# Performance work log

Hardware: AMD Instinct MI355X
Metric: run time of the kernel (lower is better)

The kernel has to match this reference:

```python
import jax, jax.numpy as jnp
import numpy as np

N_NODES = 100000
N_EDGES = 3200000
NUM_FEATURES = 512
LATENT_DIM = 64
HIDDEN = 2 * LATENT_DIM


def gcn_conv(x, src, dst, deg_inv_sqrt, W, b, n_nodes):
    # GCNConv: out = D^{-1/2} (A+I) D^{-1/2} X W + b  (transform first, then aggregate)
    h = x @ W  # [N, out]
    norm = deg_inv_sqrt[src] * deg_inv_sqrt[dst]  # [E]
    msg = h[src] * norm[:, None]  # gather + scale
    out = jax.ops.segment_sum(msg, dst, num_segments=n_nodes)
    return out + b


def setup_inputs() -> dict:
    key = jax.random.key(0)
    ks = jax.random.split(key, 8)
    features = jax.random.normal(ks[0], (N_NODES, NUM_FEATURES), dtype=jnp.float32)
    edge_index = jax.random.randint(ks[1], (2, N_EDGES), 0, N_NODES, dtype=jnp.int64)
    # Glorot-ish params
    W1 = jax.random.normal(ks[2], (NUM_FEATURES, HIDDEN), dtype=jnp.float32) / np.sqrt(NUM_FEATURES)
    b1 = jnp.zeros((HIDDEN,), dtype=jnp.float32)
    Wm = jax.random.normal(ks[3], (HIDDEN, LATENT_DIM), dtype=jnp.float32) / np.sqrt(HIDDEN)
    bm = jnp.zeros((LATENT_DIM,), dtype=jnp.float32)
    Wv = jax.random.normal(ks[4], (HIDDEN, LATENT_DIM), dtype=jnp.float32) / np.sqrt(HIDDEN)
    bv = jnp.zeros((LATENT_DIM,), dtype=jnp.float32)
    return {"features": features, "edge_index": edge_index,
            "W1": W1, "b1": b1, "Wm": Wm, "bm": bm, "Wv": Wv, "bv": bv}


def reference(features, edge_index, W1, b1, Wm, bm, Wv, bv):
    n = features.shape[0]
    loop = jnp.arange(n, dtype=edge_index.dtype)
    src = jnp.concatenate([edge_index[0], loop])  # add self-loops
    dst = jnp.concatenate([edge_index[1], loop])
    deg = jax.ops.segment_sum(jnp.ones_like(dst, dtype=features.dtype), dst, num_segments=n)
    deg_inv_sqrt = jnp.where(deg > 0, jax.lax.rsqrt(deg), 0.0)

    h = jax.nn.relu(gcn_conv(features, src, dst, deg_inv_sqrt, W1, b1, n))
    mean = gcn_conv(h, src, dst, deg_inv_sqrt, Wm, bm, n)
    var = gcn_conv(h, src, dst, deg_inv_sqrt, Wv, bv, n)
    return (mean, var)
```

## Files before the change

### kernel.cpp

```cpp
#include <hip/hip_runtime.h>

#define N_FEAT 512
#define HID 128
#define LAT 64

#define NB 98
#define BSHIFT 10
#define BS 1024
#define CAP 34816
#define CHUNK 4096

__device__ __forceinline__ unsigned short f2bf(float f) {
    unsigned u = __float_as_uint(f);
    return (unsigned short)((u + 0x7FFFu + ((u >> 16) & 1u)) >> 16);
}
__device__ __forceinline__ float bf2f(unsigned short h) {
    return __uint_as_float(((unsigned)h) << 16);
}

__global__ __launch_bounds__(256) void bin_kernel(const int* __restrict__ src,
                                                  const int* __restrict__ dst,
                                                  int* __restrict__ gcursor,
                                                  uint2* __restrict__ binned, int E) {
    __shared__ int hist[NB];
    __shared__ int basel[NB];
    __shared__ int gbase[NB];
    __shared__ int cursor[NB];
    __shared__ uint2 staged[CHUNK];
    int tid = threadIdx.x;
    int e0 = blockIdx.x * CHUNK;
    int nE = min(CHUNK, E - e0);
    if (nE <= 0) return;
    for (int i = tid; i < NB; i += 256) hist[i] = 0;
    __syncthreads();
    for (int i = tid; i < nE; i += 256) {
        int d = dst[e0 + i];
        atomicAdd(&hist[d >> BSHIFT], 1);
    }
    __syncthreads();
    if (tid < NB) basel[tid] = hist[tid];
    __syncthreads();
    for (int off = 1; off < NB; off <<= 1) {
        int x = (tid >= off && tid < NB) ? basel[tid - off] : 0;
        __syncthreads();
        if (tid < NB) basel[tid] += x;
        __syncthreads();
    }
    if (tid < NB) {
        int c = hist[tid];
        basel[tid] -= c;
        gbase[tid] = (c > 0) ? atomicAdd(&gcursor[tid], c) : 0;
        cursor[tid] = basel[tid];
    }
    __syncthreads();
    for (int i = tid; i < nE; i += 256) {
        int s = src[e0 + i];
        int d = dst[e0 + i];
        int b = d >> BSHIFT;
        int pos = atomicAdd(&cursor[b], 1);
        staged[pos] = make_uint2((unsigned)s, (unsigned)d);
    }
    __syncthreads();
    for (int i = tid; i < nE; i += 256) {
        uint2 e = staged[i];
        int b = (int)(e.y >> BSHIFT);
        int ofs = gbase[b] + (i - basel[b]);
        if (ofs < CAP) binned[(size_t)b * CAP + ofs] = e;
    }
}

__global__ __launch_bounds__(1024) void build_a_kernel(const uint2* __restrict__ binned,
                                                       const int* __restrict__ gcursor,
                                                       int* __restrict__ counts,
                                                       float* __restrict__ dis,
                                                       int* __restrict__ offsets, int N) {
    __shared__ int nh[BS];
    __shared__ int pref[BS];
    int b = blockIdx.x;
    int tid = threadIdx.x;
    int nEdges = min(gcursor[b], CAP);
    const uint2* rgn = binned + (size_t)b * CAP;
    nh[tid] = 0;
    __syncthreads();
    for (int i = tid; i < nEdges; i += 1024)
        atomicAdd(&nh[rgn[i].y & (BS - 1)], 1);
    __syncthreads();
    int v = nh[tid];
    pref[tid] = v;
    __syncthreads();
    for (int off = 1; off < BS; off <<= 1) {
        int x = (tid >= off) ? pref[tid - off] : 0;
        __syncthreads();
        pref[tid] += x;
        __syncthreads();
    }
    int excl = pref[tid] - v;
    int node = (b << BSHIFT) + tid;
    if (node < N) {
        counts[node] = v;
        dis[node] = rsqrtf((float)(v + 1));
        offsets[node] = b * CAP + excl;
    }
}

__global__ __launch_bounds__(1024) void build_b_kernel(const uint2* __restrict__ binned,
                                                       const int* __restrict__ gcursor,
                                                       const int* __restrict__ offsets,
                                                       const float* __restrict__ dis,
                                                       int2* __restrict__ pairs, int N) {
    __shared__ int cur[BS];
    int b = blockIdx.x;
    int tid = threadIdx.x;
    int nEdges = min(gcursor[b], CAP);
    const uint2* rgn = binned + (size_t)b * CAP;
    int node = (b << BSHIFT) + tid;
    cur[tid] = (node < N) ? offsets[node] : 0;
    __syncthreads();
    for (int i = tid; i < nEdges; i += 1024) {
        uint2 e = rgn[i];
        int pos = atomicAdd(&cur[e.y & (BS - 1)], 1);
        float ws = dis[e.x];
        pairs[pos] = make_int2((int)e.x, __float_as_int(ws));
    }
}

__global__ __launch_bounds__(256) void wsplit_kernel(const float* __restrict__ W,
                                                     unsigned short* __restrict__ WhT,
                                                     unsigned short* __restrict__ WlT) {
    int i = blockIdx.x * 256 + threadIdx.x;
    if (i >= N_FEAT * HID) return;
    int k = i >> 7;
    int n = i & 127;
    float w = W[i];
    unsigned short h = f2bf(w);
    float r = w - bf2f(h);
    WhT[(size_t)n * N_FEAT + k] = h;
    WlT[(size_t)n * N_FEAT + k] = f2bf(r);
}

typedef __attribute__((ext_vector_type(8))) short bf16x8;
typedef __attribute__((ext_vector_type(4))) float f32x4;

#define GM 128
#define GK 32
#define LDA 40

__global__ __launch_bounds__(256) void gemm1_mfma(const float* __restrict__ X,
                                                  const unsigned short* __restrict__ WhT,
                                                  const unsigned short* __restrict__ WlT,
                                                  unsigned short* __restrict__ Tb, int M) {
    __shared__ unsigned short Ah[GM][LDA];
    __shared__ unsigned short Al[GM][LDA];
    __shared__ unsigned short Bh[HID][LDA];
    __shared__ unsigned short Bl[HID][LDA];

    int tid = threadIdx.x;
    int row = tid >> 1;
    int c0 = (tid & 1) * 16;

    int row_g = blockIdx.x * GM + row;
    if (row_g > M - 1) row_g = M - 1;
    const float* xbase = X + (size_t)row_g * N_FEAT;
    const unsigned short* whb = WhT + (size_t)row * N_FEAT;
    const unsigned short* wlb = WlT + (size_t)row * N_FEAT;

    int wid = tid >> 6, lane = tid & 63;
    int wm = wid >> 1, wn = wid & 1;
    int lm = lane & 15;
    int lk8 = (lane >> 4) * 8;

    f32x4 acc[4][4];
    #pragma unroll
    for (int i = 0; i < 4; ++i)
        #pragma unroll
        for (int j = 0; j < 4; ++j) acc[i][j] = (f32x4){0.f, 0.f, 0.f, 0.f};

    float4 xv0 = *(const float4*)(xbase + c0);
    float4 xv1 = *(const float4*)(xbase + c0 + 4);
    float4 xv2 = *(const float4*)(xbase + c0 + 8);
    float4 xv3 = *(const float4*)(xbase + c0 + 12);
    uint4 bhv0 = *(const uint4*)(whb + c0);
    uint4 bhv1 = *(const uint4*)(whb + c0 + 8);
    uint4 blv0 = *(const uint4*)(wlb + c0);
    uint4 blv1 = *(const uint4*)(wlb + c0 + 8);

    for (int k0 = 0; k0 < N_FEAT; k0 += GK) {
        __syncthreads();
        {
            float xs[16] = {xv0.x, xv0.y, xv0.z, xv0.w, xv1.x, xv1.y, xv1.z, xv1.w,
                            xv2.x, xv2.y, xv2.z, xv2.w, xv3.x, xv3.y, xv3.z, xv3.w};
            unsigned short* arow = &Ah[row][c0];
            unsigned short* lrow = &Al[row][c0];
            #pragma unroll
            for (int j = 0; j < 16; j += 2) {
                unsigned short h0 = f2bf(xs[j]);
                unsigned short h1 = f2bf(xs[j + 1]);
                float r0 = xs[j] - bf2f(h0);
                float r1 = xs[j + 1] - bf2f(h1);
                *(unsigned*)&arow[j] = (unsigned)h0 | ((unsigned)h1 << 16);
                *(unsigned*)&lrow[j] = (unsigned)f2bf(r0) | ((unsigned)f2bf(r1) << 16);
            }
            *(uint4*)&Bh[row][c0]     = bhv0;
            *(uint4*)&Bh[row][c0 + 8] = bhv1;
            *(uint4*)&Bl[row][c0]     = blv0;
            *(uint4*)&Bl[row][c0 + 8] = blv1;
        }
        __syncthreads();
        if (k0 + GK < N_FEAT) {
            const float* xp = xbase + k0 + GK + c0;
            xv0 = *(const float4*)(xp);
            xv1 = *(const float4*)(xp + 4);
            xv2 = *(const float4*)(xp + 8);
            xv3 = *(const float4*)(xp + 12);
            bhv0 = *(const uint4*)(whb + k0 + GK + c0);
            bhv1 = *(const uint4*)(whb + k0 + GK + c0 + 8);
            blv0 = *(const uint4*)(wlb + k0 + GK + c0);
            blv1 = *(const uint4*)(wlb + k0 + GK + c0 + 8);
        }
        bf16x8 ah[4], al[4], bh[4], bl[4];
        #pragma unroll
        for (int i = 0; i < 4; ++i) {
            ah[i] = *(const bf16x8*)&Ah[wm * 64 + i * 16 + lm][lk8];
            al[i] = *(const bf16x8*)&Al[wm * 64 + i * 16 + lm][lk8];
            bh[i] = *(const bf16x8*)&Bh[wn * 64 + i * 16 + lm][lk8];
            bl[i] = *(const bf16x8*)&Bl[wn * 64 + i * 16 + lm][lk8];
        }
        #pragma unroll
        for (int i = 0; i < 4; ++i)
            #pragma unroll
            for (int j = 0; j < 4; ++j) {
                acc[i][j] = __builtin_amdgcn_mfma_f32_16x16x32_bf16(ah[i], bh[j], acc[i][j], 0, 0, 0);
                acc[i][j] = __builtin_amdgcn_mfma_f32_16x16x32_bf16(al[i], bh[j], acc[i][j], 0, 0, 0);
                acc[i][j] = __builtin_amdgcn_mfma_f32_16x16x32_bf16(ah[i], bl[j], acc[i][j], 0, 0, 0);
            }
    }

    int orow0 = blockIdx.x * GM + wm * 64 + (lane >> 4) * 4;
    int ocol0 = wn * 64 + lm;
    #pragma unroll
    for (int i = 0; i < 4; ++i)
        #pragma unroll
        for (int j = 0; j < 4; ++j)
            #pragma unroll
            for (int r = 0; r < 4; ++r) {
                int orow = orow0 + i * 16 + r;
                if (orow < M)
                    Tb[(size_t)orow * HID + ocol0 + j * 16] = f2bf(acc[i][j][r]);
            }
}

template <bool RELU_BIAS, bool OUT_BF16>
__global__ __launch_bounds__(256) void agg_kernel(const unsigned short* __restrict__ Tb,
                                                  const int2* __restrict__ pairs,
                                                  const int* __restrict__ offsets,
                                                  const int* __restrict__ counts,
                                                  const float* __restrict__ dis,
                                                  const float* __restrict__ bias,
                                                  void* __restrict__ out, int n) {
    int tid = threadIdx.x;
    int half = tid >> 5;
    int lane = tid & 31;
    int i = blockIdx.x * 8 + half;
    if (i >= n) return;
    float di = dis[i];
    int beg = offsets[i];
    int cnt = counts[i];
    const int2* ep = pairs + beg;
    ushort4 self = ((const ushort4*)(Tb + (size_t)i * HID))[lane];
    float4 acc;
    acc.x = di * bf2f(self.x); acc.y = di * bf2f(self.y);
    acc.z = di * bf2f(self.z); acc.w = di * bf2f(self.w);
    if (cnt > 0) {
        int cm1 = cnt - 1;
        int s[8]; float w[8];
        #pragma unroll
        for (int u = 0; u < 8; ++u) {
            int2 p = ep[min(u, cm1)];
            s[u] = p.x;
            w[u] = (u <= cm1) ? __int_as_float(p.y) : 0.f;
        }
        for (int j = 0; j < cnt; j += 8) {
            ushort4 v[8];
            #pragma unroll
            for (int u = 0; u < 8; ++u)
                v[u] = ((const ushort4*)(Tb + (size_t)s[u] * HID))[lane];
            int jn = j + 8;
            int sN[8]; float wN[8];
            #pragma unroll
            for (int u = 0; u < 8; ++u) {
                int2 p = ep[min(jn + u, cm1)];
                sN[u] = p.x;
                wN[u] = (jn + u <= cm1) ? __int_as_float(p.y) : 0.f;
            }
            #pragma unroll
            for (int u = 0; u < 8; ++u) {
                acc.x += w[u] * bf2f(v[u].x); acc.y += w[u] * bf2f(v[u].y);
                acc.z += w[u] * bf2f(v[u].z); acc.w += w[u] * bf2f(v[u].w);
            }
            #pragma unroll
            for (int u = 0; u < 8; ++u) { s[u] = sN[u]; w[u] = wN[u]; }
        }
    }
    acc.x *= di; acc.y *= di; acc.z *= di; acc.w *= di;
    if (RELU_BIAS) {
        float4 bv = ((const float4*)bias)[lane];
        acc.x = fmaxf(acc.x + bv.x, 0.f);
        acc.y = fmaxf(acc.y + bv.y, 0.f);
        acc.z = fmaxf(acc.z + bv.z, 0.f);
        acc.w = fmaxf(acc.w + bv.w, 0.f);
    }
    if (OUT_BF16) {
        ushort4 o = {f2bf(acc.x), f2bf(acc.y), f2bf(acc.z), f2bf(acc.w)};
        ((ushort4*)((unsigned short*)out + (size_t)i * HID))[lane] = o;
    } else {
        ((float4*)((float*)out + (size_t)i * HID))[lane] = acc;
    }
}

#define BM 64
#define BN 128
#define BK 16
__global__ __launch_bounds__(256) void gemm2_kernel(const float* __restrict__ G,
                                                    const float* __restrict__ Wm,
                                                    const float* __restrict__ bm,
                                                    const float* __restrict__ Wv,
                                                    const float* __restrict__ bv,
                                                    float* __restrict__ outm,
                                                    float* __restrict__ outv, int M) {
    __shared__ float As[BM][BK + 1];
    __shared__ float Bs[BK][BN];
    int tid = threadIdx.x;
    int block_m = blockIdx.x * BM;
    int tx = tid & 15;
    int ty = tid >> 4;

    int a_row = tid >> 2;
    int a_k4 = (tid & 3) << 2;
    int a_row_g = block_m + a_row;
    int a_row_c = a_row_g < M ? a_row_g : (M - 1);
    int b_row = tid >> 5;
    int b_col = (tid & 31) << 2;
    const float* Wsel = (b_col < 64) ? (Wm + b_col) : (Wv + (b_col - 64));

    float acc[4][8];
    #pragma unroll
    for (int i = 0; i < 4; ++i)
        #pragma unroll
        for (int j = 0; j < 8; ++j) acc[i][j] = 0.f;

    for (int k0 = 0; k0 < HID; k0 += BK) {
        float4 av = *(const float4*)&G[(size_t)a_row_c * HID + k0 + a_k4];
        float4 bv0 = *(const float4*)&Wsel[(size_t)(k0 + b_row) * LAT];
        float4 bv1 = *(const float4*)&Wsel[(size_t)(k0 + b_row + 8) * LAT];
        As[a_row][a_k4 + 0] = av.x; As[a_row][a_k4 + 1] = av.y;
        As[a_row][a_k4 + 2] = av.z; As[a_row][a_k4 + 3] = av.w;
        *(float4*)&Bs[b_row][b_col] = bv0;
        *(float4*)&Bs[b_row + 8][b_col] = bv1;
        __syncthreads();
        #pragma unroll
        for (int k = 0; k < BK; ++k) {
            float a[4];
            #pragma unroll
            for (int i = 0; i < 4; ++i) a[i] = As[ty * 4 + i][k];
            float4 bq0 = *(const float4*)&Bs[k][tx * 8];
            float4 bq1 = *(const float4*)&Bs[k][tx * 8 + 4];
            float bb[8] = {bq0.x, bq0.y, bq0.z, bq0.w, bq1.x, bq1.y, bq1.z, bq1.w};
            #pragma unroll
            for (int i = 0; i < 4; ++i)
                #pragma unroll
                for (int j = 0; j < 8; ++j) acc[i][j] += a[i] * bb[j];
        }
        __syncthreads();
    }

    int col0 = tx * 8;
    float* outsel = (col0 < 64) ? (outm + col0) : (outv + (col0 - 64));
    const float* bsel = (col0 < 64) ? (bm + col0) : (bv + (col0 - 64));
    float4 bb0 = *(const float4*)&bsel[0];
    float4 bb1 = *(const float4*)&bsel[4];
    #pragma unroll
    for (int i = 0; i < 4; ++i) {
        int row = block_m + ty * 4 + i;
        if (row < M) {
            float4 o0 = {acc[i][0] + bb0.x, acc[i][1] + bb0.y, acc[i][2] + bb0.z, acc[i][3] + bb0.w};
            float4 o1 = {acc[i][4] + bb1.x, acc[i][5] + bb1.y, acc[i][6] + bb1.z, acc[i][7] + bb1.w};
            *(float4*)&outsel[(size_t)row * LAT] = o0;
            *(float4*)&outsel[(size_t)row * LAT + 4] = o1;
        }
    }
}

extern "C" void kernel_launch(void* const* d_in, const int* in_sizes, int n_in,
                              void* d_out, int out_size, void* d_ws, size_t ws_size,
                              hipStream_t stream) {
    const float* X  = (const float*)d_in[0];
    const int* edge = (const int*)d_in[1];
    const float* W1 = (const float*)d_in[2];
    const float* b1 = (const float*)d_in[3];
    const float* Wm = (const float*)d_in[4];
    const float* bm = (const float*)d_in[5];
    const float* Wv = (const float*)d_in[6];
    const float* bv = (const float*)d_in[7];

    int N = in_sizes[0] / N_FEAT;
    int E = in_sizes[1] / 2;
    const int* srcp = edge;
    const int* dstp = edge + E;

    char* w = (char*)d_ws;
    size_t off = 0;
    auto alloc = [&](size_t bytes) -> void* {
        void* p = w + off;
        off = (off + bytes + 511) & ~(size_t)511;
        return p;
    };
    float* dis    = (float*)alloc((size_t)N * 4);
    int* counts   = (int*)alloc((size_t)N * 4);
    int* offsets  = (int*)alloc((size_t)N * 4);
    int* gcursor  = (int*)alloc((size_t)NB * 4);
    int2* pairs   = (int2*)alloc((size_t)NB * CAP * 8);
    unsigned short* tb = (unsigned short*)alloc((size_t)N * HID * 2);
    unsigned short* hb = (unsigned short*)alloc((size_t)N * HID * 2);
    unsigned short* whT = (unsigned short*)alloc((size_t)N_FEAT * HID * 2);
    unsigned short* wlT = (unsigned short*)alloc((size_t)N_FEAT * HID * 2);
    float* g      = (float*)alloc((size_t)N * HID * 4);
    uint2* binned = (uint2*)g;

    hipMemsetAsync(gcursor, 0, (size_t)NB * 4, stream);
    int nChunks = (E + CHUNK - 1) / CHUNK;
    bin_kernel<<<nChunks, 256, 0, stream>>>(srcp, dstp, gcursor, binned, E);
    build_a_kernel<<<NB, 1024, 0, stream>>>(binned, gcursor, counts, dis, offsets, N);
    build_b_kernel<<<NB, 1024, 0, stream>>>(binned, gcursor, offsets, dis, pairs, N);

    wsplit_kernel<<<(N_FEAT * HID + 255) / 256, 256, 0, stream>>>(W1, whT, wlT);
    gemm1_mfma<<<(N + GM - 1) / GM, 256, 0, stream>>>(X, whT, wlT, tb, N);
    agg_kernel<true, true><<<(N + 7) / 8, 256, 0, stream>>>(tb, pairs, offsets, counts, dis, b1, hb, N);
    agg_kernel<false, false><<<(N + 7) / 8, 256, 0, stream>>>(hb, pairs, offsets, counts, dis, nullptr, g, N);

    float* outm = (float*)d_out;
    float* outv = outm + (size_t)N * LAT;
    gemm2_kernel<<<(N + BM - 1) / BM, 256, 0, stream>>>(g, Wm, bm, Wv, bv, outm, outv, N);
}
```

Measured before the change: 764.5 us.

## Use split-bf16 MFMA for second GEMM and widen aggregation loads to 16 bytes

Replaces the fp32 SIMT second GEMM with an MFMA kernel that takes its inputs as bf16 hi/lo pairs and uses three MFMA products to approximate fp32 accuracy. The second aggregation now writes split bf16 hi/lo outputs instead of fp32, which keeps the intermediate the same size while feeding the MFMA kernel directly. Aggregation switches to 16 lanes per node with 8-element (16-byte) gathers, which halves the number of gather instructions per row. The cost is an extra small weight-split kernel, and the split-bf16 scheme carries some precision risk.

```diff
diff --git a/kernel.cpp b/kernel.cpp
--- a/kernel.cpp
+++ b/kernel.cpp
@@ -17,6 +17,10 @@
 __device__ __forceinline__ float bf2f(unsigned short h) {
     return __uint_as_float(((unsigned)h) << 16);
 }
+
+typedef __attribute__((ext_vector_type(8))) short bf16x8;
+typedef __attribute__((ext_vector_type(4))) float f32x4;
+typedef __attribute__((ext_vector_type(8))) unsigned short u16x8;
 
 __global__ __launch_bounds__(256) void bin_kernel(const int* __restrict__ src,
                                                   const int* __restrict__ dst,
@@ -138,8 +142,20 @@
     WlT[(size_t)n * N_FEAT + k] = f2bf(r);
 }
 
-typedef __attribute__((ext_vector_type(8))) short bf16x8;
-typedef __attribute__((ext_vector_type(4))) float f32x4;
+__global__ __launch_bounds__(256) void wsplit2_kernel(const float* __restrict__ Wm,
+                                                      const float* __restrict__ Wv,
+                                                      unsigned short* __restrict__ WhT2,
+                                                      unsigned short* __restrict__ WlT2) {
+    int i = blockIdx.x * 256 + threadIdx.x;
+    if (i >= HID * HID) return;
+    int k = i >> 7;
+    int n = i & 127;
+    float w = (n < 64) ? Wm[(size_t)k * LAT + n] : Wv[(size_t)k * LAT + (n - 64)];
+    unsigned short h = f2bf(w);
+    float r = w - bf2f(h);
+    WhT2[(size_t)n * HID + k] = h;
+    WlT2[(size_t)n * HID + k] = f2bf(r);
+}
 
 #define GM 128
 #define GK 32
@@ -249,27 +265,127 @@
             }
 }
 
-template <bool RELU_BIAS, bool OUT_BF16>
+__global__ __launch_bounds__(256) void gemm2_mfma(const unsigned short* __restrict__ Gh,
+                                                  const unsigned short* __restrict__ Gl,
+                                                  const unsigned short* __restrict__ WhT2,
+                                                  const unsigned short* __restrict__ WlT2,
+                                                  const float* __restrict__ bm,
+                                                  const float* __restrict__ bv,
+                                                  float* __restrict__ outm,
+                                                  float* __restrict__ outv, int M) {
+    __shared__ unsigned short Ah[GM][LDA];
+    __shared__ unsigned short Al[GM][LDA];
+    __shared__ unsigned short Bh[HID][LDA];
+    __shared__ unsigned short Bl[HID][LDA];
+
+    int tid = threadIdx.x;
+    int row = tid >> 1;
+    int c0 = (tid & 1) * 16;
+
+    int row_g = blockIdx.x * GM + row;
+    if (row_g > M - 1) row_g = M - 1;
+    const unsigned short* ghb = Gh + (size_t)row_g * HID;
+    const unsigned short* glb = Gl + (size_t)row_g * HID;
+    const unsigned short* whb = WhT2 + (size_t)row * HID;
+    const unsigned short* wlb = WlT2 + (size_t)row * HID;
+
+    int wid = tid >> 6, lane = tid & 63;
+    int wm = wid >> 1, wn = wid & 1;
+    int lm = lane & 15;
+    int lk8 = (lane >> 4) * 8;
+
+    f32x4 acc[4][4];
+    #pragma unroll
+    for (int i = 0; i < 4; ++i)
+        #pragma unroll
+        for (int j = 0; j < 4; ++j) acc[i][j] = (f32x4){0.f, 0.f, 0.f, 0.f};
+
+    uint4 ahv0 = *(const uint4*)(ghb + c0);
+    uint4 ahv1 = *(const uint4*)(ghb + c0 + 8);
+    uint4 alv0 = *(const uint4*)(glb + c0);
+    uint4 alv1 = *(const uint4*)(glb + c0 + 8);
+    uint4 bhv0 = *(const uint4*)(whb + c0);
+    uint4 bhv1 = *(const uint4*)(whb + c0 + 8);
+    uint4 blv0 = *(const uint4*)(wlb + c0);
+    uint4 blv1 = *(const uint4*)(wlb + c0 + 8);
+
+    for (int k0 = 0; k0 < HID; k0 += GK) {
+        __syncthreads();
+        *(uint4*)&Ah[row][c0]     = ahv0;
+        *(uint4*)&Ah[row][c0 + 8] = ahv1;
+        *(uint4*)&Al[row][c0]     = alv0;
+        *(uint4*)&Al[row][c0 + 8] = alv1;
+        *(uint4*)&Bh[row][c0]     = bhv0;
+        *(uint4*)&Bh[row][c0 + 8] = bhv1;
+        *(uint4*)&Bl[row][c0]     = blv0;
+        *(uint4*)&Bl[row][c0 + 8] = blv1;
+        __syncthreads();
+        if (k0 + GK < HID) {
+            ahv0 = *(const uint4*)(ghb + k0 + GK + c0);
+            ahv1 = *(const uint4*)(ghb + k0 + GK + c0 + 8);
+            alv0 = *(const uint4*)(glb + k0 + GK + c0);
+            alv1 = *(const uint4*)(glb + k0 + GK + c0 + 8);
+            bhv0 = *(const uint4*)(whb + k0 + GK + c0);
+            bhv1 = *(const uint4*)(whb + k0 + GK + c0 + 8);
+            blv0 = *(const uint4*)(wlb + k0 + GK + c0);
+            blv1 = *(const uint4*)(wlb + k0 + GK + c0 + 8);
+        }
+        bf16x8 ah[4], al[4], bh[4], bl[4];
+        #pragma unroll
+        for (int i = 0; i < 4; ++i) {
+            ah[i] = *(const bf16x8*)&Ah[wm * 64 + i * 16 + lm][lk8];
+            al[i] = *(const bf16x8*)&Al[wm * 64 + i * 16 + lm][lk8];
+            bh[i] = *(const bf16x8*)&Bh[wn * 64 + i * 16 + lm][lk8];
+            bl[i] = *(const bf16x8*)&Bl[wn * 64 + i * 16 + lm][lk8];
+        }
+        #pragma unroll
+        for (int i = 0; i < 4; ++i)
+            #pragma unroll
+            for (int j = 0; j < 4; ++j) {
+                acc[i][j] = __builtin_amdgcn_mfma_f32_16x16x32_bf16(ah[i], bh[j], acc[i][j], 0, 0, 0);
+                acc[i][j] = __builtin_amdgcn_mfma_f32_16x16x32_bf16(al[i], bh[j], acc[i][j], 0, 0, 0);
+                acc[i][j] = __builtin_amdgcn_mfma_f32_16x16x32_bf16(ah[i], bl[j], acc[i][j], 0, 0, 0);
+            }
+    }
+
+    int orow0 = blockIdx.x * GM + wm * 64 + (lane >> 4) * 4;
+    #pragma unroll
+    for (int j = 0; j < 4; ++j) {
+        int col = wn * 64 + j * 16 + lm;
+        float bb = (col < 64) ? bm[col] : bv[col - 64];
+        float* optr = (col < 64) ? (outm + col) : (outv + (col - 64));
+        #pragma unroll
+        for (int i = 0; i < 4; ++i)
+            #pragma unroll
+            for (int r = 0; r < 4; ++r) {
+                int orow = orow0 + i * 16 + r;
+                if (orow < M) optr[(size_t)orow * LAT] = acc[i][j][r] + bb;
+            }
+    }
+}
+
+template <bool RELU_BIAS, bool SPLIT_OUT>
 __global__ __launch_bounds__(256) void agg_kernel(const unsigned short* __restrict__ Tb,
                                                   const int2* __restrict__ pairs,
                                                   const int* __restrict__ offsets,
                                                   const int* __restrict__ counts,
                                                   const float* __restrict__ dis,
                                                   const float* __restrict__ bias,
-                                                  void* __restrict__ out, int n) {
+                                                  unsigned short* __restrict__ out_h,
+                                                  unsigned short* __restrict__ out_l, int n) {
     int tid = threadIdx.x;
-    int half = tid >> 5;
-    int lane = tid & 31;
-    int i = blockIdx.x * 8 + half;
+    int q = tid >> 4;
+    int lane = tid & 15;
+    int i = blockIdx.x * 16 + q;
     if (i >= n) return;
     float di = dis[i];
     int beg = offsets[i];
     int cnt = counts[i];
     const int2* ep = pairs + beg;
-    ushort4 self = ((const ushort4*)(Tb + (size_t)i * HID))[lane];
-    float4 acc;
-    acc.x = di * bf2f(self.x); acc.y = di * bf2f(self.y);
-    acc.z = di * bf2f(self.z); acc.w = di * bf2f(self.w);
+    u16x8 self = ((const u16x8*)(Tb + (size_t)i * HID))[lane];
+    float acc[8];
+    #pragma unroll
+    for (int e = 0; e < 8; ++e) acc[e] = di * bf2f(self[e]);
     if (cnt > 0) {
         int cm1 = cnt - 1;
         int s[8]; float w[8];
@@ -280,10 +396,10 @@
             w[u] = (u <= cm1) ? __int_as_float(p.y) : 0.f;
         }
         for (int j = 0; j < cnt; j += 8) {
-            ushort4 v[8];
+            u16x8 v[8];
             #pragma unroll
             for (int u = 0; u < 8; ++u)
-                v[u] = ((const ushort4*)(Tb + (size_t)s[u] * HID))[lane];
+                v[u] = ((const u16x8*)(Tb + (size_t)s[u] * HID))[lane];
             int jn = j + 8;
             int sN[8]; float wN[8];
             #pragma unroll
@@ -293,100 +409,38 @@
                 wN[u] = (jn + u <= cm1) ? __int_as_float(p.y) : 0.f;
             }
             #pragma unroll
-            for (int u = 0; u < 8; ++u) {
-                acc.x += w[u] * bf2f(v[u].x); acc.y += w[u] * bf2f(v[u].y);
-                acc.z += w[u] * bf2f(v[u].z); acc.w += w[u] * bf2f(v[u].w);
-            }
+            for (int u = 0; u < 8; ++u)
+                #pragma unroll
+                for (int e = 0; e < 8; ++e)
+                    acc[e] += w[u] * bf2f(v[u][e]);
             #pragma unroll
             for (int u = 0; u < 8; ++u) { s[u] = sN[u]; w[u] = wN[u]; }
         }
     }
-    acc.x *= di; acc.y *= di; acc.z *= di; acc.w *= di;
+    #pragma unroll
+    for (int e = 0; e < 8; ++e) acc[e] *= di;
     if (RELU_BIAS) {
-        float4 bv = ((const float4*)bias)[lane];
-        acc.x = fmaxf(acc.x + bv.x, 0.f);
-        acc.y = fmaxf(acc.y + bv.y, 0.f);
-        acc.z = fmaxf(acc.z + bv.z, 0.f);
-        acc.w = fmaxf(acc.w + bv.w, 0.f);
-    }
-    if (OUT_BF16) {
-        ushort4 o = {f2bf(acc.x), f2bf(acc.y), f2bf(acc.z), f2bf(acc.w)};
-        ((ushort4*)((unsigned short*)out + (size_t)i * HID))[lane] = o;
+        float4 bv0 = *(const float4*)(bias + lane * 8);
+        float4 bv1 = *(const float4*)(bias + lane * 8 + 4);
+        float bb[8] = {bv0.x, bv0.y, bv0.z, bv0.w, bv1.x, bv1.y, bv1.z, bv1.w};
+        #pragma unroll
+        for (int e = 0; e < 8; ++e) acc[e] = fmaxf(acc[e] + bb[e], 0.f);
+    }
+    if (!SPLIT_OUT) {
+        u16x8 o;
+        #pragma unroll
+        for (int e = 0; e < 8; ++e) o[e] = f2bf(acc[e]);
+        ((u16x8*)(out_h + (size_t)i * HID))[lane] = o;
     } else {
-        ((float4*)((float*)out + (size_t)i * HID))[lane] = acc;
-    }
-}
-
-#define BM 64
-#define BN 128
-#define BK 16
-__global__ __launch_bounds__(256) void gemm2_kernel(const float* __restrict__ G,
-                                                    const float* __restrict__ Wm,
-                                                    const float* __restrict__ bm,
-                                                    const float* __restrict__ Wv,
-                                                    const float* __restrict__ bv,
-                                                    float* __restrict__ outm,
-                                                    float* __restrict__ outv, int M) {
-    __shared__ float As[BM][BK + 1];
-    __shared__ float Bs[BK][BN];
-    int tid = threadIdx.x;
-    int block_m = blockIdx.x * BM;
-    int tx = tid & 15;
-    int ty = tid >> 4;
-
-    int a_row = tid >> 2;
-    int a_k4 = (tid & 3) << 2;
-    int a_row_g = block_m + a_row;
-    int a_row_c = a_row_g < M ? a_row_g : (M - 1);
-    int b_row = tid >> 5;
-    int b_col = (tid & 31) << 2;
-    const float* Wsel = (b_col < 64) ? (Wm + b_col) : (Wv + (b_col - 64));
-
-    float acc[4][8];
-    #pragma unroll
-    for (int i = 0; i < 4; ++i)
-        #pragma unroll
-        for (int j = 0; j < 8; ++j) acc[i][j] = 0.f;
-
-    for (int k0 = 0; k0 < HID; k0 += BK) {
-        float4 av = *(const float4*)&G[(size_t)a_row_c * HID + k0 + a_k4];
-        float4 bv0 = *(const float4*)&Wsel[(size_t)(k0 + b_row) * LAT];
-        float4 bv1 = *(const float4*)&Wsel[(size_t)(k0 + b_row + 8) * LAT];
-        As[a_row][a_k4 + 0] = av.x; As[a_row][a_k4 + 1] = av.y;
-        As[a_row][a_k4 + 2] = av.z; As[a_row][a_k4 + 3] = av.w;
-        *(float4*)&Bs[b_row][b_col] = bv0;
-        *(float4*)&Bs[b_row + 8][b_col] = bv1;
-        __syncthreads();
-        #pragma unroll
-        for (int k = 0; k < BK; ++k) {
-            float a[4];
-            #pragma unroll
-            for (int i = 0; i < 4; ++i) a[i] = As[ty * 4 + i][k];
-            float4 bq0 = *(const float4*)&Bs[k][tx * 8];
-            float4 bq1 = *(const float4*)&Bs[k][tx * 8 + 4];
-            float bb[8] = {bq0.x, bq0.y, bq0.z, bq0.w, bq1.x, bq1.y, bq1.z, bq1.w};
-            #pragma unroll
-            for (int i = 0; i < 4; ++i)
-                #pragma unroll
-                for (int j = 0; j < 8; ++j) acc[i][j] += a[i] * bb[j];
-        }
-        __syncthreads();
-    }
-
-    int col0 = tx * 8;
-    float* outsel = (col0 < 64) ? (outm + col0) : (outv + (col0 - 64));
-    const float* bsel = (col0 < 64) ? (bm + col0) : (bv + (col0 - 64));
-    float4 bb0 = *(const float4*)&bsel[0];
-    float4 bb1 = *(const float4*)&bsel[4];
-    #pragma unroll
-    for (int i = 0; i < 4; ++i) {
-        int row = block_m + ty * 4 + i;
-        if (row < M) {
-            float4 o0 = {acc[i][0] + bb0.x, acc[i][1] + bb0.y, acc[i][2] + bb0.z, acc[i][3] + bb0.w};
-            float4 o1 = {acc[i][4] + bb1.x, acc[i][5] + bb1.y, acc[i][6] + bb1.z, acc[i][7] + bb1.w};
-            *(float4*)&outsel[(size_t)row * LAT] = o0;
-            *(float4*)&outsel[(size_t)row * LAT + 4] = o1;
-        }
+        u16x8 oh, ol;
+        #pragma unroll
+        for (int e = 0; e < 8; ++e) {
+            unsigned short hh = f2bf(acc[e]);
+            oh[e] = hh;
+            ol[e] = f2bf(acc[e] - bf2f(hh));
+        }
+        ((u16x8*)(out_h + (size_t)i * HID))[lane] = oh;
+        ((u16x8*)(out_l + (size_t)i * HID))[lane] = ol;
     }
 }
 
@@ -423,8 +477,11 @@
     unsigned short* hb = (unsigned short*)alloc((size_t)N * HID * 2);
     unsigned short* whT = (unsigned short*)alloc((size_t)N_FEAT * HID * 2);
     unsigned short* wlT = (unsigned short*)alloc((size_t)N_FEAT * HID * 2);
-    float* g      = (float*)alloc((size_t)N * HID * 4);
-    uint2* binned = (uint2*)g;
+    unsigned short* whT2 = (unsigned short*)alloc((size_t)HID * HID * 2);
+    unsigned short* wlT2 = (unsigned short*)alloc((size_t)HID * HID * 2);
+    unsigned short* gh = (unsigned short*)alloc((size_t)N * HID * 2);
+    unsigned short* gl = (unsigned short*)alloc((size_t)N * HID * 2);
+    uint2* binned = (uint2*)gh;
 
     hipMemsetAsync(gcursor, 0, (size_t)NB * 4, stream);
     int nChunks = (E + CHUNK - 1) / CHUNK;
@@ -433,11 +490,12 @@
     build_b_kernel<<<NB, 1024, 0, stream>>>(binned, gcursor, offsets, dis, pairs, N);
 
     wsplit_kernel<<<(N_FEAT * HID + 255) / 256, 256, 0, stream>>>(W1, whT, wlT);
+    wsplit2_kernel<<<(HID * HID + 255) / 256, 256, 0, stream>>>(Wm, Wv, whT2, wlT2);
     gemm1_mfma<<<(N + GM - 1) / GM, 256, 0, stream>>>(X, whT, wlT, tb, N);
-    agg_kernel<true, true><<<(N + 7) / 8, 256, 0, stream>>>(tb, pairs, offsets, counts, dis, b1, hb, N);
-    agg_kernel<false, false><<<(N + 7) / 8, 256, 0, stream>>>(hb, pairs, offsets, counts, dis, nullptr, g, N);
+    agg_kernel<true, false><<<(N + 15) / 16, 256, 0, stream>>>(tb, pairs, offsets, counts, dis, b1, hb, nullptr, N);
+    agg_kernel<false, true><<<(N + 15) / 16, 256, 0, stream>>>(hb, pairs, offsets, counts, dis, nullptr, gh, gl, N);
 
     float* outm = (float*)d_out;
     float* outv = outm + (size_t)N * LAT;
-    gemm2_kernel<<<(N + BM - 1) / BM, 256, 0, stream>>>(g, Wm, bm, Wv, bv, outm, outv, N);
-}
+    gemm2_mfma<<<(N + GM - 1) / GM, 256, 0, stream>>>(gh, gl, whT2, wlT2, bm, bv, outm, outv, N);
+}
```

Measured after the change: 735.2 us. 1.04x faster.
